# Performance work log

Measured on AMD Instinct MI355X. Metric: run time of the kernel, lower is better.

## Reference

```python
import jax, jax.numpy as jnp
import numpy as np

N_NODES = 50000
N_EDGES = 1000000
HID = 64
L = 3
EPS_MSG = 1e-7   # GENConv message eps
EPS_SM = 1e-16   # PyG scatter-softmax denominator eps
LN_EPS = 1e-5


def layernorm(x, g, b):
    mu = jnp.mean(x, axis=-1, keepdims=True)
    var = jnp.var(x, axis=-1, keepdims=True)
    return (x - mu) * jax.lax.rsqrt(var + LN_EPS) * g + b


def genconv(x, src, dst, edge_attr, t, W1, b1, g1, be1, W2, b2):
    # message: relu(x_j + e_ij) + eps  -> [E, HID]
    msg = jax.nn.relu(x[src] + edge_attr) + EPS_MSG
    # softmax aggregation over incoming edges of each dst node
    logits = msg * t
    m = jax.ops.segment_max(logits, dst, num_segments=N_NODES)
    m = jnp.where(jnp.isfinite(m), m, 0.0)
    e = jnp.exp(logits - m[dst])
    s = jax.ops.segment_sum(e, dst, num_segments=N_NODES) + EPS_SM
    agg = jax.ops.segment_sum((e / s[dst]) * msg, dst, num_segments=N_NODES)
    # root residual + MLP [64 -> 128 -> 64]
    h = agg + x
    h = h @ W1 + b1
    h = jax.nn.relu(layernorm(h, g1, be1))
    return h @ W2 + b2


def setup_inputs() -> dict:
    key = jax.random.key(0)
    ks = jax.random.split(key, 10)
    inp = {
        'x': jax.random.normal(ks[0], (N_NODES, 16), jnp.float32),
        'edge_attr': jax.random.uniform(ks[1], (N_EDGES, 1), jnp.float32),
        'edge_index': jax.random.randint(ks[2], (2, N_EDGES), 0, N_NODES, jnp.int32),
        'W_node': jax.random.normal(ks[3], (16, HID), jnp.float32) / np.sqrt(16.0),
        'b_node': jnp.zeros((HID,), jnp.float32),
        'W_edge': jax.random.normal(ks[4], (1, HID), jnp.float32),
        'b_edge': jnp.zeros((HID,), jnp.float32),
        't': jnp.ones((L,), jnp.float32),
        'W1': jax.random.normal(ks[5], (L, HID, 2 * HID), jnp.float32) / np.sqrt(float(HID)),
        'b1': jnp.zeros((L, 2 * HID), jnp.float32),
        'ln_g': jnp.ones((L, 2 * HID), jnp.float32),
        'ln_b': jnp.zeros((L, 2 * HID), jnp.float32),
        'W2': jax.random.normal(ks[6], (L, 2 * HID, HID), jnp.float32) / np.sqrt(2.0 * HID),
        'b2': jnp.zeros((L, HID), jnp.float32),
        'norm_g': jnp.ones((L, HID), jnp.float32),
        'norm_b': jnp.zeros((L, HID), jnp.float32),
        'W_lin': jax.random.normal(ks[7], (HID, 64), jnp.float32) / np.sqrt(float(HID)),
        'b_lin': jnp.zeros((64,), jnp.float32),
    }
    return inp


def reference(x, edge_attr, edge_index, W_node, b_node, W_edge, b_edge, t,
              W1, b1, ln_g, ln_b, W2, b2, norm_g, norm_b, W_lin, b_lin):
    src, dst = edge_index[0], edge_index[1]
    h = x @ W_node + b_node                 # [N, HID]
    ea = edge_attr @ W_edge + b_edge        # [E, HID]
    # layer 0: conv only
    h = genconv(h, src, dst, ea, t[0], W1[0], b1[0], ln_g[0], ln_b[0], W2[0], b2[0])
    # layers 1..L-1: res+ blocks (norm -> relu -> conv -> residual); dropout is identity in eval
    for i in range(1, L):
        z = jax.nn.relu(layernorm(h, norm_g[i], norm_b[i]))
        h = h + genconv(z, src, dst, ea, t[i], W1[i], b1[i], ln_g[i], ln_b[i], W2[i], b2[i])
    # final norm/act reuses layer 0's norm
    h = jax.nn.relu(layernorm(h, norm_g[0], norm_b[0]))
    # adaptive avg/max pool (N, 64) -> (1, 32): pool over all nodes, channel bins of 2
    avg = h.mean(axis=0).reshape(32, 2).mean(axis=1)
    mx = h.max(axis=0).reshape(32, 2).max(axis=1)
    emb = jnp.concatenate([avg, mx])[None, :]   # [1, 64]
    return emb @ W_lin + b_lin                  # [1, 64]
```

## Files before the change

kernel.cpp:

```cpp
#include <hip/hip_runtime.h>
#include <math.h>

#define N_NODES 50000
#define N_EDGES 1000000
#define HID 64
#define CAP 64
#define N_TILES (N_NODES / 16)
#define NB_MLP 512
#define VB_S 72
#define UB_S 136
#define NB_ENC ((N_NODES + 3) / 4)
#define NB_WPREP ((3 * 8192 + 255) / 256)
#define NB_SCAT ((N_EDGES + 255) / 256)
static_assert(N_NODES % 16 == 0, "tile math");
static_assert(N_NODES <= 65536, "src must fit in 16 bits");

typedef __attribute__((ext_vector_type(8))) short short8;
typedef __attribute__((ext_vector_type(4))) float f32x4;

__device__ __forceinline__ unsigned short f2bf(float x) {
    unsigned u = __float_as_uint(x);
    u += 0x7FFFu + ((u >> 16) & 1u);
    return (unsigned short)(u >> 16);
}
__device__ __forceinline__ float bfbits_hi(unsigned pk) {
    return __uint_as_float(pk & 0xFFFF0000u);
}
__device__ __forceinline__ float bf2f(unsigned short v) {
    return __uint_as_float(((unsigned)v) << 16);
}
__device__ __forceinline__ unsigned addpk(unsigned a, unsigned b) {
    float lo = __uint_as_float(a << 16) + __uint_as_float(b << 16);
    float hi = __uint_as_float(a & 0xFFFF0000u) + __uint_as_float(b & 0xFFFF0000u);
    return (unsigned)f2bf(lo) | ((unsigned)f2bf(hi) << 16);
}

__global__ __launch_bounds__(256) void k_front(
    const float* __restrict__ x, const float* __restrict__ Wn,
    const float* __restrict__ bn, unsigned short* __restrict__ zb,
    const float* __restrict__ W1, const float* __restrict__ W2,
    unsigned short* __restrict__ w1p, unsigned short* __restrict__ w2p,
    const int* __restrict__ ei, const float* __restrict__ eattr,
    int* __restrict__ cnt, unsigned int* __restrict__ s_pack) {
    int b = blockIdx.x;
    if (b < NB_SCAT) {
        int i = b * 256 + threadIdx.x;
        if (i >= N_EDGES) return;
        int d = ei[N_EDGES + i];
        int p = atomicAdd(&cnt[d], 1);
        unsigned pk = ((unsigned)f2bf(eattr[i]) << 16) | (unsigned)(ei[i] & 0xFFFF);
        if (p < CAP) s_pack[d * CAP + p] = pk;
    } else if (b < NB_SCAT + NB_ENC) {
        int n = (b - NB_SCAT) * 4 + (threadIdx.x >> 6);
        int c = threadIdx.x & 63;
        if (n >= N_NODES) return;
        float acc = bn[c];
        const float* xr = x + n * 16;
        #pragma unroll
        for (int k = 0; k < 16; ++k) acc = fmaf(xr[k], Wn[k * 64 + c], acc);
        zb[n * 64 + c] = f2bf(acc);
    } else {
        int i = (b - NB_SCAT - NB_ENC) * 256 + threadIdx.x;
        if (i >= 3 * 8192) return;
        int L = i >> 13, r = i & 8191;
        int j = r & 7, lane = (r >> 3) & 63;
        int quad = lane >> 4, col = lane & 15;
        {
            int st = r >> 9;
            int s = st >> 3, t = st & 7;
            w1p[i] = f2bf(W1[L * 8192 + (s * 32 + quad * 8 + j) * 128 + t * 16 + col]);
        }
        {
            int ft = r >> 9;
            int s = ft >> 2, t = ft & 3;
            w2p[i] = f2bf(W2[L * 8192 + (s * 32 + quad * 8 + j) * 64 + t * 16 + col]);
        }
    }
}

__global__ __launch_bounds__(256) void k_agg(
    const unsigned short* __restrict__ zb, const int* __restrict__ cnt,
    const unsigned int* __restrict__ s_pack,
    const float* __restrict__ We, const float* __restrict__ be,
    const float* __restrict__ t, int layer, unsigned short* __restrict__ aggb) {
    int wid = (blockIdx.x * blockDim.x + threadIdx.x) >> 6;
    int lane = threadIdx.x & 63;
    if (wid >= N_NODES) return;
    int deg = cnt[wid];
    deg = (deg < CAP) ? deg : CAP;
    int beg = wid * CAP, end = beg + deg;
    int half = lane >> 5;
    int c2 = lane & 31;
    float we0 = We[2 * c2], we1 = We[2 * c2 + 1];
    float bv0 = be[2 * c2], bv1 = be[2 * c2 + 1];
    float tl = t[layer];
    const unsigned* zbu = (const unsigned*)zb;
    float s0 = 0.f, s1 = 0.f, n0 = 0.f, n1 = 0.f;
    int i = beg;
    for (; i + 7 < end; i += 8) {
        unsigned pk[4];
        #pragma unroll
        for (int j = 0; j < 4; ++j) {
            unsigned pa = s_pack[i + 2 * j];
            unsigned pb = s_pack[i + 2 * j + 1];
            pk[j] = half ? pb : pa;
        }
        unsigned zu[4];
        #pragma unroll
        for (int j = 0; j < 4; ++j) zu[j] = zbu[(pk[j] & 0xFFFFu) * 32 + c2];
        #pragma unroll
        for (int j = 0; j < 4; ++j) {
            float ea = bfbits_hi(pk[j]);
            float z0 = __uint_as_float(zu[j] << 16);
            float z1 = __uint_as_float(zu[j] & 0xFFFF0000u);
            float m0 = fmaxf(z0 + fmaf(ea, we0, bv0), 0.f) + 1e-7f;
            float m1 = fmaxf(z1 + fmaf(ea, we1, bv1), 0.f) + 1e-7f;
            float p0 = __expf(m0 * tl), p1 = __expf(m1 * tl);
            s0 += p0; n0 = fmaf(p0, m0, n0);
            s1 += p1; n1 = fmaf(p1, m1, n1);
        }
    }
    for (; i + 1 < end; i += 2) {
        unsigned pa = s_pack[i], pb = s_pack[i + 1];
        unsigned pk = half ? pb : pa;
        unsigned zu = zbu[(pk & 0xFFFFu) * 32 + c2];
        float ea = bfbits_hi(pk);
        float z0 = __uint_as_float(zu << 16);
        float z1 = __uint_as_float(zu & 0xFFFF0000u);
        float m0 = fmaxf(z0 + fmaf(ea, we0, bv0), 0.f) + 1e-7f;
        float m1 = fmaxf(z1 + fmaf(ea, we1, bv1), 0.f) + 1e-7f;
        float p0 = __expf(m0 * tl), p1 = __expf(m1 * tl);
        s0 += p0; n0 = fmaf(p0, m0, n0);
        s1 += p1; n1 = fmaf(p1, m1, n1);
    }
    if (i < end) {
        unsigned pk = s_pack[i];
        unsigned zu = zbu[(pk & 0xFFFFu) * 32 + c2];
        float ea = bfbits_hi(pk);
        float z0 = __uint_as_float(zu << 16);
        float z1 = __uint_as_float(zu & 0xFFFF0000u);
        float m0 = fmaxf(z0 + fmaf(ea, we0, bv0), 0.f) + 1e-7f;
        float m1 = fmaxf(z1 + fmaf(ea, we1, bv1), 0.f) + 1e-7f;
        float p0 = __expf(m0 * tl), p1 = __expf(m1 * tl);
        if (half == 0) {
            s0 += p0; n0 = fmaf(p0, m0, n0);
            s1 += p1; n1 = fmaf(p1, m1, n1);
        }
    }
    s0 += __shfl_xor(s0, 32, 64); n0 += __shfl_xor(n0, 32, 64);
    s1 += __shfl_xor(s1, 32, 64); n1 += __shfl_xor(n1, 32, 64);
    if (half == 0) {
        unsigned r = (unsigned)f2bf(n0 / (s0 + 1e-16f)) |
                     ((unsigned)f2bf(n1 / (s1 + 1e-16f)) << 16);
        ((unsigned*)aggb)[wid * 32 + c2] = r;
    }
}

__global__ __launch_bounds__(256) void k_mlp(
    const unsigned short* __restrict__ aggb, unsigned short* __restrict__ zb,
    unsigned short* __restrict__ hb,
    const unsigned short* __restrict__ w1p, const unsigned short* __restrict__ w2p,
    const float* __restrict__ b1,
    const float* __restrict__ g1, const float* __restrict__ be1,
    const float* __restrict__ b2,
    const float* __restrict__ ng, const float* __restrict__ nb, int mode,
    float* __restrict__ pb_sum, float* __restrict__ pb_max) {
    __shared__ unsigned short w1s[8192];
    __shared__ unsigned short w2s[8192];
    __shared__ unsigned short vbuf[4][16 * VB_S];
    __shared__ unsigned short ubuf[4][16 * UB_S];
    __shared__ float lssum[4][4][16], lsmax[4][4][16];
    int lane = threadIdx.x & 63;
    int wave = threadIdx.x >> 6;
    int col = lane & 15, quad = lane >> 4;
    unsigned short* vb = vbuf[wave];
    unsigned short* ub = ubuf[wave];

    {
        const uint4* s1 = (const uint4*)w1p;
        const uint4* s2 = (const uint4*)w2p;
        uint4* d1 = (uint4*)w1s;
        uint4* d2 = (uint4*)w2s;
        #pragma unroll
        for (int i = 0; i < 4; ++i) {
            d1[threadIdx.x + i * 256] = s1[threadIdx.x + i * 256];
            d2[threadIdx.x + i * 256] = s2[threadIdx.x + i * 256];
        }
    }
    __syncthreads();

    float b1f[8], g1f[8], e1f[8];
    #pragma unroll
    for (int t = 0; t < 8; ++t) {
        int ch = t * 16 + col;
        b1f[t] = b1[ch]; g1f[t] = g1[ch]; e1f[t] = be1[ch];
    }
    float b2f_[4], ngf[4], nbf[4];
    #pragma unroll
    for (int t = 0; t < 4; ++t) {
        b2f_[t] = b2[t * 16 + col];
        ngf[t] = ng[t * 16 + col];
        nbf[t] = nb[t * 16 + col];
    }

    float psum[4] = {0.f, 0.f, 0.f, 0.f};
    float pmax[4] = {0.f, 0.f, 0.f, 0.f};
    int nd = lane >> 2;
    int cg = (lane & 3) * 16;

    for (int tile = blockIdx.x * 4 + wave; tile < N_TILES; tile += NB_MLP * 4) {
        int n0 = tile * 16;
        const uint4* ap = (const uint4*)(aggb + (size_t)(n0 + nd) * 64 + cg);
        const uint4* zp = (const uint4*)(zb + (size_t)(n0 + nd) * 64 + cg);
        uint4 a0 = ap[0], a1 = ap[1], z0 = zp[0], z1 = zp[1];
        uint4 r0, r1;
        r0.x = addpk(a0.x, z0.x); r0.y = addpk(a0.y, z0.y);
        r0.z = addpk(a0.z, z0.z); r0.w = addpk(a0.w, z0.w);
        r1.x = addpk(a1.x, z1.x); r1.y = addpk(a1.y, z1.y);
        r1.z = addpk(a1.z, z1.z); r1.w = addpk(a1.w, z1.w);
        uint4* vdst = (uint4*)&vb[nd * VB_S + cg];
        vdst[0] = r0;
        vdst[1] = r1;

        short8 af0 = *(const short8*)&vb[col * VB_S + quad * 8];
        short8 af1 = *(const short8*)&vb[col * VB_S + 32 + quad * 8];

        uint4 h0, h1;
        if (mode >= 1) {
            const uint4* hp = (const uint4*)(hb + (size_t)(n0 + nd) * 64 + cg);
            h0 = hp[0]; h1 = hp[1];
        }

        f32x4 au[8];
        #pragma unroll
        for (int t = 0; t < 8; ++t) {
            short8 w0 = *(const short8*)&w1s[((0 * 8 + t) * 64 + lane) * 8];
            short8 w1 = *(const short8*)&w1s[((1 * 8 + t) * 64 + lane) * 8];
            f32x4 c = {0.f, 0.f, 0.f, 0.f};
            c = __builtin_amdgcn_mfma_f32_16x16x32_bf16(af0, w0, c, 0, 0, 0);
            c = __builtin_amdgcn_mfma_f32_16x16x32_bf16(af1, w1, c, 0, 0, 0);
            au[t] = c;
        }
        #pragma unroll
        for (int r = 0; r < 4; ++r) {
            float sx = 0.f, sq = 0.f;
            #pragma unroll
            for (int t = 0; t < 8; ++t) {
                float v = au[t][r] + b1f[t];
                sx += v; sq += v * v;
            }
            #pragma unroll
            for (int mask = 1; mask < 16; mask <<= 1) {
                sx += __shfl_xor(sx, mask, 64);
                sq += __shfl_xor(sq, mask, 64);
            }
            float mu = sx * (1.f / 128.f);
            float var = sq * (1.f / 128.f) - mu * mu;
            float rs = rsqrtf(var + 1e-5f);
            int row = quad * 4 + r;
            #pragma unroll
            for (int t = 0; t < 8; ++t) {
                float v = au[t][r] + b1f[t];
                float y = fmaxf(fmaf((v - mu) * rs, g1f[t], e1f[t]), 0.f);
                ub[row * UB_S + t * 16 + col] = f2bf(y);
            }
        }
        f32x4 oc[4];
        #pragma unroll
        for (int t = 0; t < 4; ++t) oc[t] = (f32x4){0.f, 0.f, 0.f, 0.f};
        #pragma unroll
        for (int s = 0; s < 4; ++s) {
            short8 a = *(const short8*)&ub[col * UB_S + s * 32 + quad * 8];
            #pragma unroll
            for (int t = 0; t < 4; ++t) {
                short8 w = *(const short8*)&w2s[((s * 4 + t) * 64 + lane) * 8];
                oc[t] = __builtin_amdgcn_mfma_f32_16x16x32_bf16(a, w, oc[t], 0, 0, 0);
            }
        }
        if (mode >= 1) {
            uint4* hdst = (uint4*)&vb[nd * VB_S + cg];
            hdst[0] = h0;
            hdst[1] = h1;
        }
        #pragma unroll
        for (int r = 0; r < 4; ++r) {
            int row = quad * 4 + r;
            float val[4];
            #pragma unroll
            for (int t = 0; t < 4; ++t) {
                val[t] = oc[t][r] + b2f_[t];
                if (mode >= 1) val[t] += bf2f(vb[row * VB_S + t * 16 + col]);
            }
            float sx = 0.f, sq = 0.f;
            #pragma unroll
            for (int t = 0; t < 4; ++t) { sx += val[t]; sq += val[t] * val[t]; }
            #pragma unroll
            for (int mask = 1; mask < 16; mask <<= 1) {
                sx += __shfl_xor(sx, mask, 64);
                sq += __shfl_xor(sq, mask, 64);
            }
            float mu = sx * (1.f / 64.f);
            float var = sq * (1.f / 64.f) - mu * mu;
            float rs = rsqrtf(var + 1e-5f);
            #pragma unroll
            for (int t = 0; t < 4; ++t) {
                float y = fmaxf(fmaf((val[t] - mu) * rs, ngf[t], nbf[t]), 0.f);
                if (mode <= 1) {
                    vb[row * VB_S + t * 16 + col] = f2bf(val[t]);
                    ub[row * UB_S + t * 16 + col] = f2bf(y);
                } else {
                    psum[t] += y;
                    pmax[t] = fmaxf(pmax[t], y);
                }
            }
        }
        if (mode <= 1) {
            const uint4* hsrc = (const uint4*)&vb[nd * VB_S + cg];
            const uint4* zsrc = (const uint4*)&ub[nd * UB_S + cg];
            uint4* hdst = (uint4*)(hb + (size_t)(n0 + nd) * 64 + cg);
            uint4* zdst = (uint4*)(zb + (size_t)(n0 + nd) * 64 + cg);
            hdst[0] = hsrc[0]; hdst[1] = hsrc[1];
            zdst[0] = zsrc[0]; zdst[1] = zsrc[1];
        }
    }
    if (mode == 2) {
        #pragma unroll
        for (int t = 0; t < 4; ++t) {
            psum[t] += __shfl_xor(psum[t], 16, 64);
            psum[t] += __shfl_xor(psum[t], 32, 64);
            pmax[t] = fmaxf(pmax[t], __shfl_xor(pmax[t], 16, 64));
            pmax[t] = fmaxf(pmax[t], __shfl_xor(pmax[t], 32, 64));
        }
        if (quad == 0) {
            #pragma unroll
            for (int t = 0; t < 4; ++t) {
                lssum[wave][t][col] = psum[t];
                lsmax[wave][t][col] = pmax[t];
            }
        }
        __syncthreads();
        if (wave == 0) {
            int t = lane >> 4, c = lane & 15;
            float s = lssum[0][t][c] + lssum[1][t][c] + lssum[2][t][c] + lssum[3][t][c];
            float mx = fmaxf(fmaxf(lsmax[0][t][c], lsmax[1][t][c]),
                             fmaxf(lsmax[2][t][c], lsmax[3][t][c]));
            pb_sum[blockIdx.x * 64 + lane] = s;
            pb_max[blockIdx.x * 64 + lane] = mx;
        }
    }
}

__global__ __launch_bounds__(1024) void k_head(
    const float* __restrict__ pb_sum, const float* __restrict__ pb_max,
    const float* __restrict__ Wl, const float* __restrict__ bl, float* __restrict__ out) {
    __shared__ float sa4[16][64], sm4[16][64];
    __shared__ float sa[64], sm[64], emb[64];
    int t = threadIdx.x;
    int ch = t & 63, part = t >> 6;
    float s = 0.f, mx = 0.f;
    for (int b = part; b < NB_MLP; b += 16) {
        s += pb_sum[b * 64 + ch];
        mx = fmaxf(mx, pb_max[b * 64 + ch]);
    }
    sa4[part][ch] = s; sm4[part][ch] = mx;
    __syncthreads();
    if (t < 64) {
        float ss = 0.f, mm = 0.f;
        #pragma unroll
        for (int q = 0; q < 16; ++q) {
            ss += sa4[q][t];
            mm = fmaxf(mm, sm4[q][t]);
        }
        sa[t] = ss; sm[t] = mm;
    }
    __syncthreads();
    if (t < 64) {
        if (t < 32) {
            emb[t] = (sa[2 * t] + sa[2 * t + 1]) * (0.5f / (float)N_NODES);
        } else {
            int i = t - 32;
            emb[t] = fmaxf(sm[2 * i], sm[2 * i + 1]);
        }
    }
    __syncthreads();
    if (t < 64) {
        float acc = bl[t];
        for (int k = 0; k < 64; ++k) acc = fmaf(emb[k], Wl[k * 64 + t], acc);
        out[t] = acc;
    }
}

extern "C" void kernel_launch(void* const* d_in, const int* in_sizes, int n_in,
                              void* d_out, int out_size, void* d_ws, size_t ws_size,
                              hipStream_t stream) {
    const float* x     = (const float*)d_in[0];
    const float* eattr = (const float*)d_in[1];
    const int*   ei    = (const int*)d_in[2];
    const float* Wn    = (const float*)d_in[3];
    const float* bn    = (const float*)d_in[4];
    const float* We    = (const float*)d_in[5];
    const float* be    = (const float*)d_in[6];
    const float* t     = (const float*)d_in[7];
    const float* W1    = (const float*)d_in[8];
    const float* b1    = (const float*)d_in[9];
    const float* lg    = (const float*)d_in[10];
    const float* lb    = (const float*)d_in[11];
    const float* W2    = (const float*)d_in[12];
    const float* b2    = (const float*)d_in[13];
    const float* ng    = (const float*)d_in[14];
    const float* nb    = (const float*)d_in[15];
    const float* Wl    = (const float*)d_in[16];
    const float* bl    = (const float*)d_in[17];
    float* out = (float*)d_out;

    char* p = (char*)d_ws;
    unsigned short* hb   = (unsigned short*)p; p += (size_t)N_NODES * 64 * 2;
    unsigned short* zb   = (unsigned short*)p; p += (size_t)N_NODES * 64 * 2;
    unsigned short* aggb = (unsigned short*)p; p += (size_t)N_NODES * 64 * 2;
    unsigned int* s_pack = (unsigned int*)p; p += (size_t)N_NODES * CAP * 4;
    int* cnt    = (int*)p;  p += (size_t)N_NODES * 4;
    float* pb_sum = (float*)p; p += (size_t)NB_MLP * 64 * 4;
    float* pb_max = (float*)p; p += (size_t)NB_MLP * 64 * 4;
    unsigned short* w1p = (unsigned short*)p; p += (size_t)3 * 8192 * 2;
    unsigned short* w2p = (unsigned short*)p; p += (size_t)3 * 8192 * 2;

    hipMemsetAsync(cnt, 0, (size_t)N_NODES * sizeof(int), stream);

    k_front<<<NB_SCAT + NB_ENC + NB_WPREP, 256, 0, stream>>>(
        x, Wn, bn, zb, W1, W2, w1p, w2p, ei, eattr, cnt, s_pack);

    k_agg<<<(N_NODES + 3) / 4, 256, 0, stream>>>(zb, cnt, s_pack, We, be, t, 0, aggb);
    k_mlp<<<NB_MLP, 256, 0, stream>>>(aggb, zb, hb, w1p, w2p, b1, lg, lb, b2,
                                      ng + 64, nb + 64, 0, pb_sum, pb_max);
    k_agg<<<(N_NODES + 3) / 4, 256, 0, stream>>>(zb, cnt, s_pack, We, be, t, 1, aggb);
    k_mlp<<<NB_MLP, 256, 0, stream>>>(aggb, zb, hb, w1p + 8192, w2p + 8192,
                                      b1 + 128, lg + 128, lb + 128, b2 + 64,
                                      ng + 128, nb + 128, 1, pb_sum, pb_max);
    k_agg<<<(N_NODES + 3) / 4, 256, 0, stream>>>(zb, cnt, s_pack, We, be, t, 2, aggb);
    k_mlp<<<NB_MLP, 256, 0, stream>>>(aggb, zb, hb, w1p + 2 * 8192, w2p + 2 * 8192,
                                      b1 + 2 * 128, lg + 2 * 128, lb + 2 * 128, b2 + 2 * 64,
                                      ng, nb, 2, pb_sum, pb_max);

    k_head<<<1, 1024, 0, stream>>>(pb_sum, pb_max, Wl, bl, out);
}
```

Measured before the change: 325.9 us.

## Replace global-atomic edge scatter with two-pass shared-memory bucket sort

The per-edge global atomicAdd scatter into per-node slots is replaced by a two-level counting sort. The first pass bins edges into coarse 256-node buckets using block-local histograms and shared-memory reordering, then writes them out contiguously. The second pass sorts each bucket by node in shared memory and writes coalesced per-node slot lists. This cuts global atomic contention and scattered writes, at the cost of an extra kernel launch, an intermediate coarse buffer, and a bucket capacity limit (BKCAP) that could drop edges if a bucket overflows.

```diff
diff --git a/kernel.cpp b/kernel.cpp
--- a/kernel.cpp
+++ b/kernel.cpp
@@ -11,7 +11,10 @@
 #define UB_S 136
 #define NB_ENC ((N_NODES + 3) / 4)
 #define NB_WPREP ((3 * 8192 + 255) / 256)
-#define NB_SCAT ((N_EDGES + 255) / 256)
+#define NBK 196
+#define BKCAP 6144
+#define EPB 4096
+#define NB1 ((N_EDGES + EPB - 1) / EPB)
 static_assert(N_NODES % 16 == 0, "tile math");
 static_assert(N_NODES <= 65536, "src must fit in 16 bits");
 
@@ -39,19 +42,10 @@
     const float* __restrict__ x, const float* __restrict__ Wn,
     const float* __restrict__ bn, unsigned short* __restrict__ zb,
     const float* __restrict__ W1, const float* __restrict__ W2,
-    unsigned short* __restrict__ w1p, unsigned short* __restrict__ w2p,
-    const int* __restrict__ ei, const float* __restrict__ eattr,
-    int* __restrict__ cnt, unsigned int* __restrict__ s_pack) {
+    unsigned short* __restrict__ w1p, unsigned short* __restrict__ w2p) {
     int b = blockIdx.x;
-    if (b < NB_SCAT) {
-        int i = b * 256 + threadIdx.x;
-        if (i >= N_EDGES) return;
-        int d = ei[N_EDGES + i];
-        int p = atomicAdd(&cnt[d], 1);
-        unsigned pk = ((unsigned)f2bf(eattr[i]) << 16) | (unsigned)(ei[i] & 0xFFFF);
-        if (p < CAP) s_pack[d * CAP + p] = pk;
-    } else if (b < NB_SCAT + NB_ENC) {
-        int n = (b - NB_SCAT) * 4 + (threadIdx.x >> 6);
+    if (b < NB_ENC) {
+        int n = b * 4 + (threadIdx.x >> 6);
         int c = threadIdx.x & 63;
         if (n >= N_NODES) return;
         float acc = bn[c];
@@ -60,7 +54,7 @@
         for (int k = 0; k < 16; ++k) acc = fmaf(xr[k], Wn[k * 64 + c], acc);
         zb[n * 64 + c] = f2bf(acc);
     } else {
-        int i = (b - NB_SCAT - NB_ENC) * 256 + threadIdx.x;
+        int i = (b - NB_ENC) * 256 + threadIdx.x;
         if (i >= 3 * 8192) return;
         int L = i >> 13, r = i & 8191;
         int j = r & 7, lane = (r >> 3) & 63;
@@ -75,6 +69,109 @@
             int s = ft >> 2, t = ft & 3;
             w2p[i] = f2bf(W2[L * 8192 + (s * 32 + quad * 8 + j) * 64 + t * 16 + col]);
         }
+    }
+}
+
+__global__ __launch_bounds__(256) void k_bin1(
+    const int* __restrict__ ei, const float* __restrict__ eattr,
+    int* __restrict__ gcnt, uint2* __restrict__ coarse) {
+    __shared__ unsigned pk_l[EPB];
+    __shared__ unsigned short dst_l[EPB];
+    __shared__ unsigned spk[EPB];
+    __shared__ unsigned short sdst[EPB];
+    __shared__ int hist[NBK], loc[NBK], gbase[NBK], cur[NBK];
+    __shared__ int inc[256];
+    int tid = threadIdx.x;
+    int e0 = blockIdx.x * EPB;
+    int nel = N_EDGES - e0; if (nel > EPB) nel = EPB;
+    for (int b = tid; b < NBK; b += 256) { hist[b] = 0; cur[b] = 0; }
+    __syncthreads();
+    for (int j = tid; j < nel; j += 256) {
+        int i = e0 + j;
+        int d = ei[N_EDGES + i];
+        unsigned pk = ((unsigned)f2bf(eattr[i]) << 16) | (unsigned)(ei[i] & 0xFFFF);
+        pk_l[j] = pk; dst_l[j] = (unsigned short)d;
+        atomicAdd(&hist[d >> 8], 1);
+    }
+    __syncthreads();
+    int v = (tid < NBK) ? hist[tid] : 0;
+    inc[tid] = v;
+    __syncthreads();
+    #pragma unroll
+    for (int dd = 1; dd < 256; dd <<= 1) {
+        int t2 = (tid >= dd) ? inc[tid - dd] : 0;
+        __syncthreads();
+        inc[tid] += t2;
+        __syncthreads();
+    }
+    if (tid < NBK) {
+        loc[tid] = inc[tid] - v;
+        gbase[tid] = atomicAdd(&gcnt[tid], v);
+    }
+    __syncthreads();
+    for (int j = tid; j < nel; j += 256) {
+        int bkt = dst_l[j] >> 8;
+        int r = atomicAdd(&cur[bkt], 1);
+        int pos = loc[bkt] + r;
+        spk[pos] = pk_l[j]; sdst[pos] = dst_l[j];
+    }
+    __syncthreads();
+    for (int j = tid; j < nel; j += 256) {
+        int d = sdst[j];
+        int bkt = d >> 8;
+        int off = gbase[bkt] + (j - loc[bkt]);
+        if (off < BKCAP) coarse[(size_t)bkt * BKCAP + off] = make_uint2(spk[j], (unsigned)d);
+    }
+}
+
+__global__ __launch_bounds__(256) void k_bin2(
+    const int* __restrict__ gcnt, const uint2* __restrict__ coarse,
+    int* __restrict__ cnt, unsigned int* __restrict__ s_pack) {
+    __shared__ unsigned epk[BKCAP];
+    __shared__ unsigned char eln[BKCAP];
+    __shared__ unsigned spk[BKCAP];
+    __shared__ unsigned char sln[BKCAP];
+    __shared__ int hist[256], cur[256], inc2[256];
+    int tid = threadIdx.x;
+    int b = blockIdx.x;
+    int m = gcnt[b]; if (m > BKCAP) m = BKCAP;
+    hist[tid] = 0; cur[tid] = 0;
+    __syncthreads();
+    for (int j = tid; j < m; j += 256) {
+        uint2 e = coarse[(size_t)b * BKCAP + j];
+        epk[j] = e.x;
+        int ln = (int)(e.y & 255u);
+        eln[j] = (unsigned char)ln;
+        atomicAdd(&hist[ln], 1);
+    }
+    __syncthreads();
+    int v = hist[tid];
+    inc2[tid] = v;
+    __syncthreads();
+    #pragma unroll
+    for (int dd = 1; dd < 256; dd <<= 1) {
+        int t2 = (tid >= dd) ? inc2[tid - dd] : 0;
+        __syncthreads();
+        inc2[tid] += t2;
+        __syncthreads();
+    }
+    int lv = inc2[tid] - v;
+    __syncthreads();
+    hist[tid] = lv;
+    int node = b * 256 + tid;
+    if (node < N_NODES) cnt[node] = v;
+    __syncthreads();
+    for (int j = tid; j < m; j += 256) {
+        int ln = eln[j];
+        int r = atomicAdd(&cur[ln], 1);
+        int pos = hist[ln] + r;
+        spk[pos] = epk[j]; sln[pos] = (unsigned char)ln;
+    }
+    __syncthreads();
+    for (int j = tid; j < m; j += 256) {
+        int ln = sln[j];
+        int k = j - hist[ln];
+        if (k < CAP) s_pack[(size_t)(b * 256 + ln) * CAP + k] = spk[j];
     }
 }
 
@@ -419,15 +516,18 @@
     unsigned short* aggb = (unsigned short*)p; p += (size_t)N_NODES * 64 * 2;
     unsigned int* s_pack = (unsigned int*)p; p += (size_t)N_NODES * CAP * 4;
     int* cnt    = (int*)p;  p += (size_t)N_NODES * 4;
+    int* gcnt   = (int*)p;  p += (size_t)256 * 4;
+    uint2* coarse = (uint2*)p; p += (size_t)NBK * BKCAP * 8;
     float* pb_sum = (float*)p; p += (size_t)NB_MLP * 64 * 4;
     float* pb_max = (float*)p; p += (size_t)NB_MLP * 64 * 4;
     unsigned short* w1p = (unsigned short*)p; p += (size_t)3 * 8192 * 2;
     unsigned short* w2p = (unsigned short*)p; p += (size_t)3 * 8192 * 2;
 
-    hipMemsetAsync(cnt, 0, (size_t)N_NODES * sizeof(int), stream);
-
-    k_front<<<NB_SCAT + NB_ENC + NB_WPREP, 256, 0, stream>>>(
-        x, Wn, bn, zb, W1, W2, w1p, w2p, ei, eattr, cnt, s_pack);
+    hipMemsetAsync(gcnt, 0, (size_t)NBK * sizeof(int), stream);
+
+    k_front<<<NB_ENC + NB_WPREP, 256, 0, stream>>>(x, Wn, bn, zb, W1, W2, w1p, w2p);
+    k_bin1<<<NB1, 256, 0, stream>>>(ei, eattr, gcnt, coarse);
+    k_bin2<<<NBK, 256, 0, stream>>>(gcnt, coarse, cnt, s_pack);
 
     k_agg<<<(N_NODES + 3) / 4, 256, 0, stream>>>(zb, cnt, s_pack, We, be, t, 0, aggb);
     k_mlp<<<NB_MLP, 256, 0, stream>>>(aggb, zb, hb, w1p, w2p, b1, lg, lb, b2,
```

After: 297.5 us, median of 2. -8.7%, faster.
